# Kernel tuning notes

Hardware: AMD Instinct MI355X
Metric: run time of the kernel (lower is better)

## Reference

```python
import jax, jax.numpy as jnp
import numpy as np

B, C, N, T, H = 4, 128, 512, 16, 4
DK = C // H
SCALE = float(np.sqrt(DK) * 1.0)  # dk**0.5 * max(tau,1e-6), tau=1.0


def setup_inputs() -> dict:
    key = jax.random.key(0)
    ks = jax.random.split(key, 6)
    x = jax.random.normal(ks[0], (B, C, N, T), jnp.float32)
    Wq = jax.random.normal(ks[1], (C, C), jnp.float32) * (1.0 / np.sqrt(C))
    Wk = jax.random.normal(ks[2], (C, C), jnp.float32) * (1.0 / np.sqrt(C))
    # original init is identity; add tiny noise so it's not degenerate
    structural = jnp.eye(N, dtype=jnp.float32) + 0.01 * jax.random.normal(ks[3], (N, N), jnp.float32)
    fusion_w = jax.random.normal(ks[4], (2,), jnp.float32) * 0.5  # 1x1 conv over 2 input channels
    fusion_b = (jax.random.normal(ks[5], (), jnp.float32) * 0.1)
    return {"x": x, "Wq": Wq, "Wk": Wk, "structural": structural,
            "fusion_w": fusion_w, "fusion_b": fusion_b}


def reference(x, Wq, Wk, structural, fusion_w, fusion_b):
    # x: [B, C, N, T]. 1x1 conv == per-channel linear; arrange to [B,T,N,H,DK]
    Q = jnp.einsum('oc,bcnt->btno', Wq, x).reshape(B, T, N, H, DK)
    K = jnp.einsum('oc,bcnt->btno', Wk, x).reshape(B, T, N, H, DK)
    # scores: [B, T, H, N, N]
    scores = jnp.einsum('btnhd,btmhd->bthnm', Q, K) / SCALE
    att_node = jax.nn.softmax(scores, axis=-1).mean(axis=(1, 2))  # [B, N, N]
    att_struct = jax.nn.softmax(structural, axis=-1)              # [N, N]
    # fusion conv (1x1, 2->1 channels) == weighted sum + bias
    fused = fusion_w[0] * att_node + fusion_w[1] * att_struct[None] + fusion_b
    fused = 0.5 * (fused + jnp.swapaxes(fused, 1, 2))  # symmetrize
    fused = jax.nn.softmax(fused, axis=-1)             # normalize='softmax'
    x_bt = jnp.transpose(x, (0, 3, 2, 1))              # [B, T, N, C]
    x_att = jnp.einsum('bij,btjc->btic', fused, x_bt)  # weighted aggregation over nodes
    return jnp.transpose(x_att, (0, 3, 2, 1))          # [B, C, N, T]
```

## Files before the change

kernel.cpp:

```cpp
#include <hip/hip_runtime.h>

#define BB 4
#define CC 128
#define NN 512
#define TT 16
#define HH 4
#define DKK 32
#define INV_SCALE 0.17677669529663687f

typedef __attribute__((ext_vector_type(8))) short bf16x8;
typedef __attribute__((ext_vector_type(4))) float f32x4;

__device__ __forceinline__ unsigned int pk2bf(float a, float b) {
  unsigned int ua = __float_as_uint(a);
  ua = (ua + 0x7FFFu + ((ua >> 16) & 1u)) >> 16;
  unsigned int ub = __float_as_uint(b);
  ub = (ub + 0x7FFFu + ((ub >> 16) & 1u)) >> 16;
  return ua | (ub << 16);
}

__device__ __forceinline__ ushort cv1(float f) {
  unsigned int u = __float_as_uint(f);
  return (ushort)((u + 0x7FFFu + ((u >> 16) & 1u)) >> 16);
}

__device__ __forceinline__ unsigned int pkfast(float a, float b) {
  unsigned int au = __float_as_uint(a) + 0x8000u;
  unsigned int bu = __float_as_uint(b) + 0x8000u;
  return __builtin_amdgcn_perm(bu, au, 0x07060302u);
}

__global__ __launch_bounds__(256) void k_wconv(const float* __restrict__ Wq,
                                               const float* __restrict__ Wk,
                                               ushort* __restrict__ Wqb,
                                               ushort* __restrict__ Wkb) {
  const int gid = blockIdx.x * 256 + threadIdx.x;
  const int i = gid * 4;
  const float* src = (i < 16384) ? (Wq + i) : (Wk + i - 16384);
  ushort* dst = (i < 16384) ? (Wqb + i) : (Wkb + i - 16384);
  float4 v = *(const float4*)src;
  uint2 u;
  u.x = pk2bf(v.x, v.y);
  u.y = pk2bf(v.z, v.w);
  *(uint2*)dst = u;
}

__global__ __launch_bounds__(256) void k_proj(const float* __restrict__ x,
                                              const ushort* __restrict__ Wqb,
                                              const ushort* __restrict__ Wkb,
                                              ushort* __restrict__ Qb,
                                              ushort* __restrict__ Kb) {
  __shared__ float xl[128 * 128];
  const int b = blockIdx.y;
  const int nt0 = blockIdx.x * 128;
  const int tid = threadIdx.x;
  const int w = tid >> 6, lane = tid & 63;
  const int lm = lane & 15, quad = lane >> 4;

  const float* xb = x + (size_t)b * 1048576 + nt0;
#pragma unroll
  for (int L = tid * 4; L < 16384; L += 1024) {
    int c = L >> 7, j = L & 127;
    *(float4*)(xl + L) = *(const float4*)(xb + c * 8192 + j);
  }

  const int o0 = w * 32;
  bf16x8 aq[2][4], ak[2][4];
#pragma unroll
  for (int ot = 0; ot < 2; ++ot)
#pragma unroll
    for (int kc = 0; kc < 4; ++kc) {
      int off = (o0 + ot * 16 + lm) * 128 + kc * 32 + quad * 8;
      aq[ot][kc] = *(const bf16x8*)(Wqb + off);
      ak[ot][kc] = *(const bf16x8*)(Wkb + off);
    }
  __syncthreads();

  const int nq = nt0 >> 4;
#pragma unroll 2
  for (int jt = 0; jt < 8; ++jt) {
    bf16x8 bfr[4];
#pragma unroll
    for (int kc = 0; kc < 4; ++kc) {
      const float* sp = xl + (kc * 32 + quad * 8) * 128 + jt * 16 + lm;
      float f0 = sp[0],   f1 = sp[128], f2 = sp[256], f3 = sp[384];
      float f4 = sp[512], f5 = sp[640], f6 = sp[768], f7 = sp[896];
      uint4 u;
      u.x = pkfast(f0, f1);
      u.y = pkfast(f2, f3);
      u.z = pkfast(f4, f5);
      u.w = pkfast(f6, f7);
      union { uint4 u; bf16x8 v; } cv;
      cv.u = u;
      bfr[kc] = cv.v;
    }

    f32x4 accq0 = {0,0,0,0}, accq1 = {0,0,0,0};
    f32x4 acck0 = {0,0,0,0}, acck1 = {0,0,0,0};
#pragma unroll
    for (int kc = 0; kc < 4; ++kc) {
      accq0 = __builtin_amdgcn_mfma_f32_16x16x32_bf16(aq[0][kc], bfr[kc], accq0, 0, 0, 0);
      accq1 = __builtin_amdgcn_mfma_f32_16x16x32_bf16(aq[1][kc], bfr[kc], accq1, 0, 0, 0);
      acck0 = __builtin_amdgcn_mfma_f32_16x16x32_bf16(ak[0][kc], bfr[kc], acck0, 0, 0, 0);
      acck1 = __builtin_amdgcn_mfma_f32_16x16x32_bf16(ak[1][kc], bfr[kc], acck1, 0, 0, 0);
    }

    const size_t base = (size_t)b * 1048576 + (size_t)lm * 65536 + w * 16384 +
                        (size_t)(nq + jt) * 32 + quad * 4;
    uint2 uq0, uq1, uk0, uk1;
    uq0.x = pk2bf(accq0[0], accq0[1]); uq0.y = pk2bf(accq0[2], accq0[3]);
    uq1.x = pk2bf(accq1[0], accq1[1]); uq1.y = pk2bf(accq1[2], accq1[3]);
    uk0.x = pk2bf(acck0[0], acck0[1]); uk0.y = pk2bf(acck0[2], acck0[3]);
    uk1.x = pk2bf(acck1[0], acck1[1]); uk1.y = pk2bf(acck1[2], acck1[3]);
    *(uint2*)(Qb + base)      = uq0;
    *(uint2*)(Qb + base + 16) = uq1;
    *(uint2*)(Kb + base)      = uk0;
    *(uint2*)(Kb + base + 16) = uk1;
  }
}

__global__ __launch_bounds__(256, 4) void k_scores(const ushort* __restrict__ Qb,
                                                   const ushort* __restrict__ Kb,
                                                   ushort* __restrict__ part) {
  __shared__ float SH[16 * 516];
  __shared__ float red[2][4][16];
  const int strip = blockIdx.x, g = blockIdx.y, b = blockIdx.z;
  const int tid = threadIdx.x;
  const int w = tid >> 6, lane = tid & 63;
  const int lm = lane & 15, quad = lane >> 4;
  const int n0 = strip * 16;
  const int wcol0 = w * 128;

  float acc[32];
#pragma unroll
  for (int i = 0; i < 32; ++i) acc[i] = 0.f;

  for (int pi = 0; pi < 8; ++pi) {
    const int p = (g << 3) + pi;
    const size_t base = (size_t)((b * 16 + (p >> 2)) * 4 + (p & 3)) * 16384;
    bf16x8 afrag = *(const bf16x8*)(Qb + base + (size_t)(n0 + lm) * 32 + quad * 8);
    bf16x8 bfr[8];
#pragma unroll
    for (int ct = 0; ct < 8; ++ct)
      bfr[ct] = *(const bf16x8*)(Kb + base + (size_t)(wcol0 + ct * 16 + lm) * 32 + quad * 8);

    f32x4 d[8];
#pragma unroll
    for (int ct = 0; ct < 8; ++ct) {
      f32x4 z = {0.f, 0.f, 0.f, 0.f};
      d[ct] = __builtin_amdgcn_mfma_f32_16x16x32_bf16(afrag, bfr[ct], z, 0, 0, 0);
    }

    float cur[32];
    float rp0 = 0.f, rp1 = 0.f, rp2 = 0.f, rp3 = 0.f;
#pragma unroll
    for (int ct = 0; ct < 8; ++ct) {
      float e0 = __expf(d[ct][0] * INV_SCALE);
      float e1 = __expf(d[ct][1] * INV_SCALE);
      float e2 = __expf(d[ct][2] * INV_SCALE);
      float e3 = __expf(d[ct][3] * INV_SCALE);
      cur[ct * 4 + 0] = e0; cur[ct * 4 + 1] = e1;
      cur[ct * 4 + 2] = e2; cur[ct * 4 + 3] = e3;
      rp0 += e0; rp1 += e1; rp2 += e2; rp3 += e3;
    }
#pragma unroll
    for (int m = 1; m < 16; m <<= 1) {
      rp0 += __shfl_xor(rp0, m);
      rp1 += __shfl_xor(rp1, m);
      rp2 += __shfl_xor(rp2, m);
      rp3 += __shfl_xor(rp3, m);
    }
    if (lm == 0) {
      red[pi & 1][w][quad * 4 + 0] = rp0;
      red[pi & 1][w][quad * 4 + 1] = rp1;
      red[pi & 1][w][quad * 4 + 2] = rp2;
      red[pi & 1][w][quad * 4 + 3] = rp3;
    }
    __syncthreads();
#pragma unroll
    for (int r = 0; r < 4; ++r) {
      float rs = red[pi & 1][0][quad * 4 + r] + red[pi & 1][1][quad * 4 + r] +
                 red[pi & 1][2][quad * 4 + r] + red[pi & 1][3][quad * 4 + r];
      float inv = 1.0f / rs;
#pragma unroll
      for (int ct = 0; ct < 8; ++ct)
        acc[ct * 4 + r] = fmaf(cur[ct * 4 + r], inv, acc[ct * 4 + r]);
    }
  }

#pragma unroll
  for (int ct = 0; ct < 8; ++ct) {
#pragma unroll
    for (int r = 0; r < 4; ++r)
      SH[(quad * 4 + r) * 516 + wcol0 + ct * 16 + lm] = acc[ct * 4 + r];
  }
  __syncthreads();
  const int row = tid >> 4, colb = (tid & 15) * 4;
  ushort* po = part + ((size_t)((g * 4 + b) * 512 + n0 + row)) * 512 + colb;
#pragma unroll
  for (int k = 0; k < 8; ++k) {
    f32x4 v = *(const f32x4*)(SH + row * 516 + colb + k * 64);
    uint2 u;
    u.x = pk2bf(v[0], v[1]);
    u.y = pk2bf(v[2], v[3]);
    *(uint2*)(po + k * 64) = u;
  }
}

__global__ __launch_bounds__(256) void k_reduce(const ushort* __restrict__ part,
                                                float* __restrict__ accA) {
  const int gid = blockIdx.x * 256 + threadIdx.x;
  const size_t idx = (size_t)gid * 4;
  float s0 = 0.f, s1 = 0.f, s2 = 0.f, s3 = 0.f;
#pragma unroll
  for (int g = 0; g < 8; ++g) {
    ushort4 v = *(const ushort4*)(part + (size_t)g * 1048576 + idx);
    s0 += __uint_as_float((unsigned int)v.x << 16);
    s1 += __uint_as_float((unsigned int)v.y << 16);
    s2 += __uint_as_float((unsigned int)v.z << 16);
    s3 += __uint_as_float((unsigned int)v.w << 16);
  }
  float4 o = make_float4(s0, s1, s2, s3);
  *(float4*)(accA + idx) = o;
}

__global__ __launch_bounds__(256) void k_sym(float* __restrict__ accA,
                                             float* __restrict__ st) {
  __shared__ float L1[64 * 68];
  __shared__ float L2[64 * 68];
  const int z = blockIdx.y;
  float* M = (z < 4) ? (accA + (size_t)z * 262144) : st;
  int rem = blockIdx.x, ti = 0;
  for (;;) { int cnt = 8 - ti; if (rem < cnt) break; rem -= cnt; ++ti; }
  const int tj = ti + rem;
  const bool diag = (ti == tj);
  const int tid = threadIdx.x;

#pragma unroll
  for (int it = 0; it < 4; ++it) {
    int L = tid * 4 + it * 1024;
    int r = L >> 6, c = L & 63;
    *(float4*)(L1 + r * 68 + c) = *(const float4*)(M + (ti * 64 + r) * 512 + tj * 64 + c);
    if (!diag)
      *(float4*)(L2 + r * 68 + c) = *(const float4*)(M + (tj * 64 + r) * 512 + ti * 64 + c);
  }
  __syncthreads();

  const float* LT = diag ? L1 : L2;
#pragma unroll
  for (int it = 0; it < 4; ++it) {
    int L = tid * 4 + it * 1024;
    int r = L >> 6, c = L & 63;
    float4 o1;
    o1.x = L1[r * 68 + c + 0] + LT[(c + 0) * 68 + r];
    o1.y = L1[r * 68 + c + 1] + LT[(c + 1) * 68 + r];
    o1.z = L1[r * 68 + c + 2] + LT[(c + 2) * 68 + r];
    o1.w = L1[r * 68 + c + 3] + LT[(c + 3) * 68 + r];
    *(float4*)(M + (ti * 64 + r) * 512 + tj * 64 + c) = o1;
    if (!diag) {
      float4 o2;
      o2.x = L2[r * 68 + c + 0] + L1[(c + 0) * 68 + r];
      o2.y = L2[r * 68 + c + 1] + L1[(c + 1) * 68 + r];
      o2.z = L2[r * 68 + c + 2] + L1[(c + 2) * 68 + r];
      o2.w = L2[r * 68 + c + 3] + L1[(c + 3) * 68 + r];
      *(float4*)(M + (tj * 64 + r) * 512 + ti * 64 + c) = o2;
    }
  }
}

__global__ __launch_bounds__(256) void k_xconv(const float* __restrict__ x,
                                               ushort* __restrict__ xtb) {
  __shared__ ushort xs[16 * 520];
  const int c = blockIdx.x, b = blockIdx.y;
  const int tid = threadIdx.x;
  const float* in = x + ((size_t)b * 128 + c) * 8192;
  ushort* outp = xtb + ((size_t)b * 128 + c) * 8192;

#pragma unroll
  for (int it = 0; it < 8; ++it) {
    int idx = (tid + it * 256) * 4;
    int j = idx >> 4, t0 = idx & 15;
    float4 v = *(const float4*)(in + idx);
    xs[(t0 + 0) * 520 + j] = cv1(v.x);
    xs[(t0 + 1) * 520 + j] = cv1(v.y);
    xs[(t0 + 2) * 520 + j] = cv1(v.z);
    xs[(t0 + 3) * 520 + j] = cv1(v.w);
  }
  __syncthreads();
#pragma unroll
  for (int it = 0; it < 4; ++it) {
    int u = (tid + it * 256) * 8;
    int t = u >> 9, j0 = u & 511;
    *(uint4*)(outp + u) = *(const uint4*)(xs + t * 520 + j0);
  }
}

__device__ __forceinline__ float blk_max(float v, float* red, int tid) {
#pragma unroll
  for (int off = 32; off > 0; off >>= 1) v = fmaxf(v, __shfl_xor(v, off, 64));
  if ((tid & 63) == 0) red[tid >> 6] = v;
  __syncthreads();
  v = fmaxf(fmaxf(red[0], red[1]), fmaxf(red[2], red[3]));
  __syncthreads();
  return v;
}
__device__ __forceinline__ float blk_sum(float v, float* red, int tid) {
#pragma unroll
  for (int off = 32; off > 0; off >>= 1) v += __shfl_xor(v, off, 64);
  if ((tid & 63) == 0) red[tid >> 6] = v;
  __syncthreads();
  v = (red[0] + red[1]) + (red[2] + red[3]);
  __syncthreads();
  return v;
}

__global__ __launch_bounds__(256) void k_struct(const float* __restrict__ S,
                                                float* __restrict__ st) {
  __shared__ float red[4];
  const int i = blockIdx.x, tid = threadIdx.x;
  float s0 = S[i * 512 + tid], s1 = S[i * 512 + tid + 256];
  float m = blk_max(fmaxf(s0, s1), red, tid);
  float e0 = __expf(s0 - m), e1 = __expf(s1 - m);
  float sum = blk_sum(e0 + e1, red, tid);
  float inv = 1.0f / sum;
  st[i * 512 + tid] = e0 * inv;
  st[i * 512 + tid + 256] = e1 * inv;
}

__global__ __launch_bounds__(256) void k_fused(const float* __restrict__ accA,
                                               const float* __restrict__ st,
                                               const float* __restrict__ fw,
                                               const float* __restrict__ fb,
                                               ushort* __restrict__ fusedb) {
  __shared__ float red[4];
  const int i = blockIdx.x, b = blockIdx.y, tid = threadIdx.x;
  const float w0s = fw[0] * (0.5f / 64.f);
  const float w1s = fw[1] * 0.5f;
  const float bias = fb[0];
  const float* A = accA + (size_t)b * 262144 + (size_t)i * 512;
  const float* S = st + (size_t)i * 512;
  float2 a2 = *(const float2*)(A + tid * 2);
  float2 s2 = *(const float2*)(S + tid * 2);
  float l0 = fmaf(w0s, a2.x, fmaf(w1s, s2.x, bias));
  float l1 = fmaf(w0s, a2.y, fmaf(w1s, s2.y, bias));
  float m = blk_max(fmaxf(l0, l1), red, tid);
  float e0 = __expf(l0 - m), e1 = __expf(l1 - m);
  float sum = blk_sum(e0 + e1, red, tid);
  float inv = 1.0f / sum;
  *(unsigned int*)(fusedb + ((size_t)(b * 512 + i)) * 512 + tid * 2) =
      pk2bf(e0 * inv, e1 * inv);
}

__global__ __launch_bounds__(256) void k_agg(const ushort* __restrict__ fusedb,
                                             const ushort* __restrict__ xtb,
                                             float* __restrict__ out) {
  __shared__ ushort xs[16 * 520];
  const int cg = blockIdx.x;
  const int i0 = blockIdx.y * 64;
  const int b = blockIdx.z;
  const int tid = threadIdx.x, w = tid >> 6, lane = tid & 63;
  const int lm = lane & 15, quad = lane >> 4;

  const ushort* fr = fusedb + ((size_t)(b * 512 + i0 + w * 16 + lm)) * 512 + quad * 8;
  bf16x8 af[16];
#pragma unroll
  for (int kk = 0; kk < 16; ++kk) af[kk] = *(const bf16x8*)(fr + kk * 32);

  const ushort* xg = xtb + ((size_t)b * 128 + cg * 8) * 8192;
  uint4 rg[4];
#pragma unroll
  for (int it = 0; it < 4; ++it) rg[it] = *(const uint4*)(xg + (tid + it * 256) * 8);

  for (int c = 0; c < 8; ++c) {
#pragma unroll
    for (int it = 0; it < 4; ++it) {
      int u = (tid + it * 256) * 8;
      int t = u >> 9, j0 = u & 511;
      *(uint4*)(xs + t * 520 + j0) = rg[it];
    }
    __syncthreads();
    if (c < 7) {
      const ushort* xg2 = xg + (size_t)(c + 1) * 8192;
#pragma unroll
      for (int it = 0; it < 4; ++it) rg[it] = *(const uint4*)(xg2 + (tid + it * 256) * 8);
    }
    f32x4 acc = {0.f, 0.f, 0.f, 0.f};
#pragma unroll
    for (int kk = 0; kk < 16; ++kk) {
      bf16x8 bf = *(const bf16x8*)(xs + lm * 520 + kk * 32 + quad * 8);
      acc = __builtin_amdgcn_mfma_f32_16x16x32_bf16(af[kk], bf, acc, 0, 0, 0);
    }
    float* op = out + (size_t)b * 1048576 + (size_t)(cg * 8 + c) * 8192 +
                (size_t)(i0 + w * 16 + quad * 4) * 16 + lm;
    op[0]  = acc[0];
    op[16] = acc[1];
    op[32] = acc[2];
    op[48] = acc[3];
    __syncthreads();
  }
}

extern "C" void kernel_launch(void* const* d_in, const int* in_sizes, int n_in,
                              void* d_out, int out_size, void* d_ws, size_t ws_size,
                              hipStream_t stream) {
  const float* x  = (const float*)d_in[0];
  const float* Wq = (const float*)d_in[1];
  const float* Wk = (const float*)d_in[2];
  const float* S  = (const float*)d_in[3];
  const float* fw = (const float*)d_in[4];
  const float* fb = (const float*)d_in[5];
  float* out = (float*)d_out;

  ushort* Qb   = (ushort*)d_ws;
  ushort* Kb   = Qb + 4194304;
  ushort* part = Kb + 4194304;
  ushort* xtb  = (ushort*)d_ws;
  float* accA  = (float*)d_ws + 8388608;
  float* st    = accA + 1048576;
  ushort* fusedb = (ushort*)(st + 262144);
  ushort* Wqb  = fusedb + 1048576;
  ushort* Wkb  = Wqb + 16384;

  k_wconv <<<dim3(32),        256, 0, stream>>>(Wq, Wk, Wqb, Wkb);
  k_proj  <<<dim3(64, 4),     256, 0, stream>>>(x, Wqb, Wkb, Qb, Kb);
  k_scores<<<dim3(32, 8, 4),  256, 0, stream>>>(Qb, Kb, part);
  k_struct<<<dim3(512),       256, 0, stream>>>(S, st);
  k_reduce<<<dim3(1024),      256, 0, stream>>>(part, accA);
  k_sym   <<<dim3(36, 5),     256, 0, stream>>>(accA, st);
  k_xconv <<<dim3(128, 4),    256, 0, stream>>>(x, xtb);
  k_fused <<<dim3(512, 4),    256, 0, stream>>>(accA, st, fw, fb, fusedb);
  k_agg   <<<dim3(16, 8, 4),  256, 0, stream>>>(fusedb, xtb, out);
}
```

Before: 161.8 us.

## Fuse pipeline stages to cut kernel launches from nine to five

Folds the weight bf16 conversion into the projection kernel. Halves the score partial groups from 8 to 4, so each block accumulates 16 (t,h) pairs. Merges the partial reduction with symmetrization and the structural softmax (which now writes a transposed copy), and merges the x transpose-convert with the fused softmax kernel. The aim is to save launch overhead and partial-buffer traffic, at the cost of fewer score blocks in flight and longer per-block loops.

```diff
diff --git a/kernel.cpp b/kernel.cpp
--- a/kernel.cpp
+++ b/kernel.cpp
@@ -30,24 +30,9 @@
   return __builtin_amdgcn_perm(bu, au, 0x07060302u);
 }
 
-__global__ __launch_bounds__(256) void k_wconv(const float* __restrict__ Wq,
-                                               const float* __restrict__ Wk,
-                                               ushort* __restrict__ Wqb,
-                                               ushort* __restrict__ Wkb) {
-  const int gid = blockIdx.x * 256 + threadIdx.x;
-  const int i = gid * 4;
-  const float* src = (i < 16384) ? (Wq + i) : (Wk + i - 16384);
-  ushort* dst = (i < 16384) ? (Wqb + i) : (Wkb + i - 16384);
-  float4 v = *(const float4*)src;
-  uint2 u;
-  u.x = pk2bf(v.x, v.y);
-  u.y = pk2bf(v.z, v.w);
-  *(uint2*)dst = u;
-}
-
 __global__ __launch_bounds__(256) void k_proj(const float* __restrict__ x,
-                                              const ushort* __restrict__ Wqb,
-                                              const ushort* __restrict__ Wkb,
+                                              const float* __restrict__ Wq,
+                                              const float* __restrict__ Wk,
                                               ushort* __restrict__ Qb,
                                               ushort* __restrict__ Kb) {
   __shared__ float xl[128 * 128];
@@ -71,8 +56,17 @@
 #pragma unroll
     for (int kc = 0; kc < 4; ++kc) {
       int off = (o0 + ot * 16 + lm) * 128 + kc * 32 + quad * 8;
-      aq[ot][kc] = *(const bf16x8*)(Wqb + off);
-      ak[ot][kc] = *(const bf16x8*)(Wkb + off);
+      float4 q0 = *(const float4*)(Wq + off);
+      float4 q1 = *(const float4*)(Wq + off + 4);
+      float4 k0 = *(const float4*)(Wk + off);
+      float4 k1 = *(const float4*)(Wk + off + 4);
+      union { uint4 u; bf16x8 v; } cq, ck;
+      cq.u = make_uint4(pk2bf(q0.x, q0.y), pk2bf(q0.z, q0.w),
+                        pk2bf(q1.x, q1.y), pk2bf(q1.z, q1.w));
+      ck.u = make_uint4(pk2bf(k0.x, k0.y), pk2bf(k0.z, k0.w),
+                        pk2bf(k1.x, k1.y), pk2bf(k1.z, k1.w));
+      aq[ot][kc] = cq.v;
+      ak[ot][kc] = ck.v;
     }
   __syncthreads();
 
@@ -135,8 +129,8 @@
 #pragma unroll
   for (int i = 0; i < 32; ++i) acc[i] = 0.f;
 
-  for (int pi = 0; pi < 8; ++pi) {
-    const int p = (g << 3) + pi;
+  for (int pi = 0; pi < 16; ++pi) {
+    const int p = (g << 4) + pi;
     const size_t base = (size_t)((b * 16 + (p >> 2)) * 4 + (p & 3)) * 16384;
     bf16x8 afrag = *(const bf16x8*)(Qb + base + (size_t)(n0 + lm) * 32 + quad * 8);
     bf16x8 bfr[8];
@@ -207,46 +201,108 @@
   }
 }
 
-__global__ __launch_bounds__(256) void k_reduce(const ushort* __restrict__ part,
-                                                float* __restrict__ accA) {
-  const int gid = blockIdx.x * 256 + threadIdx.x;
-  const size_t idx = (size_t)gid * 4;
-  float s0 = 0.f, s1 = 0.f, s2 = 0.f, s3 = 0.f;
-#pragma unroll
-  for (int g = 0; g < 8; ++g) {
-    ushort4 v = *(const ushort4*)(part + (size_t)g * 1048576 + idx);
-    s0 += __uint_as_float((unsigned int)v.x << 16);
-    s1 += __uint_as_float((unsigned int)v.y << 16);
-    s2 += __uint_as_float((unsigned int)v.z << 16);
-    s3 += __uint_as_float((unsigned int)v.w << 16);
-  }
-  float4 o = make_float4(s0, s1, s2, s3);
-  *(float4*)(accA + idx) = o;
-}
-
-__global__ __launch_bounds__(256) void k_sym(float* __restrict__ accA,
-                                             float* __restrict__ st) {
-  __shared__ float L1[64 * 68];
-  __shared__ float L2[64 * 68];
-  const int z = blockIdx.y;
-  float* M = (z < 4) ? (accA + (size_t)z * 262144) : st;
+__global__ __launch_bounds__(256) void k_redsym(const ushort* __restrict__ part,
+                                                const float* __restrict__ S,
+                                                float* __restrict__ accS,
+                                                float* __restrict__ st,
+                                                float* __restrict__ stT) {
+  __shared__ float LBUF[8704];
+  const int tid = threadIdx.x;
+
+  if (blockIdx.y == 4) {
+    if (blockIdx.x >= 32) return;
+    float* const sh = LBUF;
+    const int i0 = blockIdx.x * 16;
+    const int w = tid >> 6, lane = tid & 63;
+#pragma unroll
+    for (int rr = 0; rr < 4; ++rr) {
+      const int r = w * 4 + rr;
+      const float* Sp = S + (size_t)(i0 + r) * 512 + lane * 8;
+      float4 a = *(const float4*)Sp;
+      float4 c = *(const float4*)(Sp + 4);
+      float m = fmaxf(fmaxf(fmaxf(a.x, a.y), fmaxf(a.z, a.w)),
+                      fmaxf(fmaxf(c.x, c.y), fmaxf(c.z, c.w)));
+#pragma unroll
+      for (int off = 32; off > 0; off >>= 1) m = fmaxf(m, __shfl_xor(m, off));
+      float e0 = __expf(a.x - m), e1 = __expf(a.y - m);
+      float e2 = __expf(a.z - m), e3 = __expf(a.w - m);
+      float e4 = __expf(c.x - m), e5 = __expf(c.y - m);
+      float e6 = __expf(c.z - m), e7 = __expf(c.w - m);
+      float s = ((e0 + e1) + (e2 + e3)) + ((e4 + e5) + (e6 + e7));
+#pragma unroll
+      for (int off = 32; off > 0; off >>= 1) s += __shfl_xor(s, off);
+      float inv = 1.0f / s;
+      float4 o1 = make_float4(e0 * inv, e1 * inv, e2 * inv, e3 * inv);
+      float4 o2 = make_float4(e4 * inv, e5 * inv, e6 * inv, e7 * inv);
+      float* op = st + (size_t)(i0 + r) * 512 + lane * 8;
+      *(float4*)op = o1;
+      *(float4*)(op + 4) = o2;
+      float* shr = sh + r * 520 + lane * 8;
+      *(float4*)shr = o1;
+      *(float4*)(shr + 4) = o2;
+    }
+    __syncthreads();
+#pragma unroll
+    for (int pp = 0; pp < 2; ++pp) {
+      const int j = tid + pp * 256;
+      float4 t0 = make_float4(sh[0 * 520 + j],  sh[1 * 520 + j],
+                              sh[2 * 520 + j],  sh[3 * 520 + j]);
+      float4 t1 = make_float4(sh[4 * 520 + j],  sh[5 * 520 + j],
+                              sh[6 * 520 + j],  sh[7 * 520 + j]);
+      float4 t2 = make_float4(sh[8 * 520 + j],  sh[9 * 520 + j],
+                              sh[10 * 520 + j], sh[11 * 520 + j]);
+      float4 t3 = make_float4(sh[12 * 520 + j], sh[13 * 520 + j],
+                              sh[14 * 520 + j], sh[15 * 520 + j]);
+      float* op = stT + (size_t)j * 512 + i0;
+      *(float4*)(op + 0)  = t0;
+      *(float4*)(op + 4)  = t1;
+      *(float4*)(op + 8)  = t2;
+      *(float4*)(op + 12) = t3;
+    }
+    return;
+  }
+
+  float* const L1 = LBUF;
+  float* const L2 = LBUF + 4352;
+  const int b = blockIdx.y;
   int rem = blockIdx.x, ti = 0;
   for (;;) { int cnt = 8 - ti; if (rem < cnt) break; rem -= cnt; ++ti; }
   const int tj = ti + rem;
   const bool diag = (ti == tj);
-  const int tid = threadIdx.x;
 
 #pragma unroll
   for (int it = 0; it < 4; ++it) {
     int L = tid * 4 + it * 1024;
     int r = L >> 6, c = L & 63;
-    *(float4*)(L1 + r * 68 + c) = *(const float4*)(M + (ti * 64 + r) * 512 + tj * 64 + c);
-    if (!diag)
-      *(float4*)(L2 + r * 68 + c) = *(const float4*)(M + (tj * 64 + r) * 512 + ti * 64 + c);
+    const ushort* p1 = part + ((size_t)b * 512 + ti * 64 + r) * 512 + tj * 64 + c;
+    float s0 = 0.f, s1 = 0.f, s2 = 0.f, s3 = 0.f;
+#pragma unroll
+    for (int g = 0; g < 4; ++g) {
+      ushort4 v = *(const ushort4*)(p1 + (size_t)g * 1048576);
+      s0 += __uint_as_float((unsigned int)v.x << 16);
+      s1 += __uint_as_float((unsigned int)v.y << 16);
+      s2 += __uint_as_float((unsigned int)v.z << 16);
+      s3 += __uint_as_float((unsigned int)v.w << 16);
+    }
+    *(float4*)(L1 + r * 68 + c) = make_float4(s0, s1, s2, s3);
+    if (!diag) {
+      const ushort* p2 = part + ((size_t)b * 512 + tj * 64 + r) * 512 + ti * 64 + c;
+      float u0 = 0.f, u1 = 0.f, u2 = 0.f, u3 = 0.f;
+#pragma unroll
+      for (int g = 0; g < 4; ++g) {
+        ushort4 v = *(const ushort4*)(p2 + (size_t)g * 1048576);
+        u0 += __uint_as_float((unsigned int)v.x << 16);
+        u1 += __uint_as_float((unsigned int)v.y << 16);
+        u2 += __uint_as_float((unsigned int)v.z << 16);
+        u3 += __uint_as_float((unsigned int)v.w << 16);
+      }
+      *(float4*)(L2 + r * 68 + c) = make_float4(u0, u1, u2, u3);
+    }
   }
   __syncthreads();
 
   const float* LT = diag ? L1 : L2;
+  float* M = accS + (size_t)b * 262144;
 #pragma unroll
   for (int it = 0; it < 4; ++it) {
     int L = tid * 4 + it * 1024;
@@ -268,33 +324,6 @@
   }
 }
 
-__global__ __launch_bounds__(256) void k_xconv(const float* __restrict__ x,
-                                               ushort* __restrict__ xtb) {
-  __shared__ ushort xs[16 * 520];
-  const int c = blockIdx.x, b = blockIdx.y;
-  const int tid = threadIdx.x;
-  const float* in = x + ((size_t)b * 128 + c) * 8192;
-  ushort* outp = xtb + ((size_t)b * 128 + c) * 8192;
-
-#pragma unroll
-  for (int it = 0; it < 8; ++it) {
-    int idx = (tid + it * 256) * 4;
-    int j = idx >> 4, t0 = idx & 15;
-    float4 v = *(const float4*)(in + idx);
-    xs[(t0 + 0) * 520 + j] = cv1(v.x);
-    xs[(t0 + 1) * 520 + j] = cv1(v.y);
-    xs[(t0 + 2) * 520 + j] = cv1(v.z);
-    xs[(t0 + 3) * 520 + j] = cv1(v.w);
-  }
-  __syncthreads();
-#pragma unroll
-  for (int it = 0; it < 4; ++it) {
-    int u = (tid + it * 256) * 8;
-    int t = u >> 9, j0 = u & 511;
-    *(uint4*)(outp + u) = *(const uint4*)(xs + t * 520 + j0);
-  }
-}
-
 __device__ __forceinline__ float blk_max(float v, float* red, int tid) {
 #pragma unroll
   for (int off = 32; off > 0; off >>= 1) v = fmaxf(v, __shfl_xor(v, off, 64));
@@ -314,35 +343,53 @@
   return v;
 }
 
-__global__ __launch_bounds__(256) void k_struct(const float* __restrict__ S,
-                                                float* __restrict__ st) {
+__global__ __launch_bounds__(256) void k_fusedx(const float* __restrict__ accS,
+                                                const float* __restrict__ st,
+                                                const float* __restrict__ stT,
+                                                const float* __restrict__ fw,
+                                                const float* __restrict__ fb,
+                                                const float* __restrict__ x,
+                                                ushort* __restrict__ fusedb,
+                                                ushort* __restrict__ xtb) {
+  __shared__ ushort xs[16 * 520];
   __shared__ float red[4];
-  const int i = blockIdx.x, tid = threadIdx.x;
-  float s0 = S[i * 512 + tid], s1 = S[i * 512 + tid + 256];
-  float m = blk_max(fmaxf(s0, s1), red, tid);
-  float e0 = __expf(s0 - m), e1 = __expf(s1 - m);
-  float sum = blk_sum(e0 + e1, red, tid);
-  float inv = 1.0f / sum;
-  st[i * 512 + tid] = e0 * inv;
-  st[i * 512 + tid + 256] = e1 * inv;
-}
-
-__global__ __launch_bounds__(256) void k_fused(const float* __restrict__ accA,
-                                               const float* __restrict__ st,
-                                               const float* __restrict__ fw,
-                                               const float* __restrict__ fb,
-                                               ushort* __restrict__ fusedb) {
-  __shared__ float red[4];
-  const int i = blockIdx.x, b = blockIdx.y, tid = threadIdx.x;
+  const int tid = threadIdx.x;
+  const int b = blockIdx.y;
+
+  if (blockIdx.x >= 512) {
+    const int c = blockIdx.x - 512;
+    const float* in = x + ((size_t)b * 128 + c) * 8192;
+    ushort* outp = xtb + ((size_t)b * 128 + c) * 8192;
+#pragma unroll
+    for (int it = 0; it < 8; ++it) {
+      int idx = (tid + it * 256) * 4;
+      int j = idx >> 4, t0 = idx & 15;
+      float4 v = *(const float4*)(in + idx);
+      xs[(t0 + 0) * 520 + j] = cv1(v.x);
+      xs[(t0 + 1) * 520 + j] = cv1(v.y);
+      xs[(t0 + 2) * 520 + j] = cv1(v.z);
+      xs[(t0 + 3) * 520 + j] = cv1(v.w);
+    }
+    __syncthreads();
+#pragma unroll
+    for (int it = 0; it < 4; ++it) {
+      int u = (tid + it * 256) * 8;
+      int t = u >> 9, j0 = u & 511;
+      *(uint4*)(outp + u) = *(const uint4*)(xs + t * 520 + j0);
+    }
+    return;
+  }
+
+  const int i = blockIdx.x;
   const float w0s = fw[0] * (0.5f / 64.f);
   const float w1s = fw[1] * 0.5f;
   const float bias = fb[0];
-  const float* A = accA + (size_t)b * 262144 + (size_t)i * 512;
-  const float* S = st + (size_t)i * 512;
+  const float* A = accS + (size_t)b * 262144 + (size_t)i * 512;
   float2 a2 = *(const float2*)(A + tid * 2);
-  float2 s2 = *(const float2*)(S + tid * 2);
-  float l0 = fmaf(w0s, a2.x, fmaf(w1s, s2.x, bias));
-  float l1 = fmaf(w0s, a2.y, fmaf(w1s, s2.y, bias));
+  float2 s2 = *(const float2*)(st + (size_t)i * 512 + tid * 2);
+  float2 t2 = *(const float2*)(stT + (size_t)i * 512 + tid * 2);
+  float l0 = fmaf(w0s, a2.x, fmaf(w1s, s2.x + t2.x, bias));
+  float l1 = fmaf(w0s, a2.y, fmaf(w1s, s2.y + t2.y, bias));
   float m = blk_max(fmaxf(l0, l1), red, tid);
   float e0 = __expf(l0 - m), e1 = __expf(l1 - m);
   float sum = blk_sum(e0 + e1, red, tid);
@@ -415,19 +462,14 @@
   ushort* Kb   = Qb + 4194304;
   ushort* part = Kb + 4194304;
   ushort* xtb  = (ushort*)d_ws;
-  float* accA  = (float*)d_ws + 8388608;
-  float* st    = accA + 1048576;
-  ushort* fusedb = (ushort*)(st + 262144);
-  ushort* Wqb  = fusedb + 1048576;
-  ushort* Wkb  = Wqb + 16384;
-
-  k_wconv <<<dim3(32),        256, 0, stream>>>(Wq, Wk, Wqb, Wkb);
-  k_proj  <<<dim3(64, 4),     256, 0, stream>>>(x, Wqb, Wkb, Qb, Kb);
-  k_scores<<<dim3(32, 8, 4),  256, 0, stream>>>(Qb, Kb, part);
-  k_struct<<<dim3(512),       256, 0, stream>>>(S, st);
-  k_reduce<<<dim3(1024),      256, 0, stream>>>(part, accA);
-  k_sym   <<<dim3(36, 5),     256, 0, stream>>>(accA, st);
-  k_xconv <<<dim3(128, 4),    256, 0, stream>>>(x, xtb);
-  k_fused <<<dim3(512, 4),    256, 0, stream>>>(accA, st, fw, fb, fusedb);
-  k_agg   <<<dim3(16, 8, 4),  256, 0, stream>>>(fusedb, xtb, out);
-}
+  float*  accS = (float*)((char*)d_ws + 25165824);
+  float*  st   = accS + 1048576;
+  float*  stT  = st + 262144;
+  ushort* fusedb = (ushort*)(stT + 262144);
+
+  k_proj  <<<dim3(64, 4),    256, 0, stream>>>(x, Wq, Wk, Qb, Kb);
+  k_scores<<<dim3(32, 4, 4), 256, 0, stream>>>(Qb, Kb, part);
+  k_redsym<<<dim3(36, 5),    256, 0, stream>>>(part, S, accS, st, stT);
+  k_fusedx<<<dim3(640, 4),   256, 0, stream>>>(accS, st, stT, fw, fb, x, fusedb, xtb);
+  k_agg   <<<dim3(16, 8, 4), 256, 0, stream>>>(fusedb, xtb, out);
+}
```

Measured after the change: 161.1 us. Within noise of the previous version (-0.4%).
